# Kernel tuning notes

Measured on AMD Instinct MI355X. Metric: run time of the kernel, lower is better.

The kernel has to match this reference:

```python
import jax, jax.numpy as jnp
import numpy as np

N = 8000        # nodes
DIN = 128       # input feature dim
DOUT = 256      # internal width (dout=128 doubled by agg='weightedmean')
HEADS = 4
MAXD = 32       # max out-degree
NEG = -1e30


def setup_inputs() -> dict:
    key = jax.random.key(0)
    ks = jax.random.split(key, 12)
    # deterministic irregular degrees: 8..32, mean 20 -> m = 160000 edges
    degs = 8 + (np.arange(N) % 25)
    m = int(degs.sum())
    e0 = np.repeat(np.arange(N), degs).astype(np.int32)        # sorted source ids
    starts = np.cumsum(degs) - degs
    pos = (np.arange(m) - np.repeat(starts, degs)).astype(np.int32)  # slot within group
    rng = np.random.default_rng(0)
    e1 = rng.integers(0, N, m).astype(np.int32)                # destination ids
    p = lambda k, sh: jax.random.normal(k, sh, jnp.float32) * 0.05
    return {
        "x": jax.random.normal(ks[0], (N, DIN), jnp.float32),
        "Wc": p(ks[1], (DOUT, 2 * DIN)), "bc": p(ks[2], (DOUT,)),
        "Wq": p(ks[3], (DOUT, DOUT)), "bq": p(ks[4], (DOUT,)),
        "Wk": p(ks[5], (DOUT, DOUT)), "bk": p(ks[6], (DOUT,)),
        "Wv": p(ks[7], (DOUT, DOUT)), "bv": p(ks[8], (DOUT,)),
        "Wo": p(ks[9], (DOUT, DOUT)), "bo": p(ks[10], (DOUT,)),
        "e0": jnp.asarray(e0), "e1": jnp.asarray(e1), "pos": jnp.asarray(pos),
        "max_deg": MAXD,
    }


def reference(x, Wc, bc, Wq, bq, Wk, bk, Wv, bv, Wo, bo, e0, e1, pos, max_deg):
    n = x.shape[0]
    m = e0.shape[0]
    H = HEADS
    dh = DOUT // H                      # head dim (64)
    # gather-concat-MLP: per-edge features
    ex = jnp.concatenate([x[e0], x[e1]], axis=1)             # [m, 2*din]
    ex = jax.nn.gelu(ex @ Wc.T + bc, approximate=False)       # [m, DOUT]
    # to_dense_batch: group edges by source node (e0 is sorted)
    dense = jnp.zeros((n, max_deg, DOUT), ex.dtype).at[e0, pos].set(ex)
    mask = jnp.zeros((n, max_deg), bool).at[e0, pos].set(True)
    # standard multi-head self-attention per node-group with key padding mask
    scale = 1.0 / jnp.sqrt(jnp.asarray(dh, ex.dtype))
    q = ((dense @ Wq.T + bq) * scale).reshape(n, max_deg, H, dh)
    k = (dense @ Wk.T + bk).reshape(n, max_deg, H, dh)
    v = (dense @ Wv.T + bv).reshape(n, max_deg, H, dh)
    scores = jnp.einsum('nqhd,nkhd->nhqk', q, k)              # [n,H,D,D]
    scores = jnp.where(mask[:, None, None, :], scores, NEG)
    attn = jax.nn.softmax(scores, axis=-1)
    out = jnp.einsum('nhqk,nkhd->nqhd', attn, v).reshape(n, max_deg, DOUT)
    out = out @ Wo.T + bo
    h = jax.nn.gelu(out[e0, pos], approximate=False)          # back to [m, DOUT]
    # weightedmean aggregation: per-head value/gate split + scatter softmax on e0
    h = h.reshape(m, H, 2, dh // 2)                           # [m,H,2,32]
    logits = h[:, :, 1].mean(axis=-1)                         # [m,H]
    gmax = jax.ops.segment_max(logits, e0, num_segments=n)    # [n,H]
    ew = jnp.exp(logits - gmax[e0])
    denom = jax.ops.segment_sum(ew, e0, num_segments=n)
    alpha = ew / denom[e0]                                    # [m,H]
    contrib = (h[:, :, 0] * alpha[:, :, None]).reshape(m, -1) # [m, H*32]
    return jax.ops.segment_sum(contrib, e1, num_segments=n)   # [n, 128]
```

## Files before the change

### kernel.cpp

```cpp
#include <hip/hip_runtime.h>
#include <math.h>

typedef unsigned short ushort_t;
typedef __attribute__((ext_vector_type(8))) short short8;
typedef __attribute__((ext_vector_type(4))) short short4_t;
typedef __attribute__((ext_vector_type(4))) float f32x4;

#define MFMA_BF16(a,b,c) __builtin_amdgcn_mfma_f32_16x16x32_bf16((a),(b),(c),0,0,0)

__device__ __forceinline__ ushort_t f2bf(float f){
  union { float f; unsigned int i; } v; v.f = f;
  unsigned int r = v.i + 0x7fffu + ((v.i >> 16) & 1u);
  return (ushort_t)(r >> 16);
}
__device__ __forceinline__ float gelu_f(float x){
  float z  = x * 0.70710678118654752f;
  float az = fabsf(z);
  float t  = __builtin_amdgcn_rcpf(1.0f + 0.3275911f * az);
  float p  = t * (0.254829592f + t * (-0.284496736f + t * (1.421413741f
             + t * (-1.453152027f + t * 1.061405429f))));
  float e  = __expf(-az * az);
  float er = 1.0f - p * e;
  er = copysignf(er, z);
  return 0.5f * x * (1.0f + er);
}
__device__ __forceinline__ short8 cvt8(const float* __restrict__ p){
  f32x4 a = *(const f32x4*)p;
  f32x4 b = *(const f32x4*)(p + 4);
  short8 t;
#pragma unroll
  for (int j = 0; j < 4; ++j) { t[j] = (short)f2bf(a[j]); t[4 + j] = (short)f2bf(b[j]); }
  return t;
}

__global__ void k_prep(const int* __restrict__ e0, const int* __restrict__ pos,
                       int m, int* __restrict__ startp, int* __restrict__ degp){
  int i = blockIdx.x * 256 + threadIdx.x;
  if (i >= m) return;
  int s = e0[i];
  if (pos[i] == 0) startp[s] = i;
  if (i == m - 1 || e0[i + 1] != s) degp[s] = pos[i] + 1;
}

__global__ void k_wcvt(const float* __restrict__ Wc, const float* __restrict__ Wq,
                       const float* __restrict__ Wk, const float* __restrict__ Wv,
                       const float* __restrict__ Wo, ushort_t* __restrict__ wb){
  int i = blockIdx.x * 256 + threadIdx.x;
  if (i >= 5 * 65536) return;
  int s = i >> 16, off = i & 65535;
  const float* src = (s == 0) ? Wc : (s == 1) ? Wq : (s == 2) ? Wk : (s == 3) ? Wv : Wo;
  wb[i] = f2bf(src[off]);
}

template<bool WB>
__global__ __launch_bounds__(256, 1) void k_fused5(
    const float* __restrict__ x,
    const ushort_t* __restrict__ wb,
    const float* __restrict__ Wcf, const float* __restrict__ bc,
    const float* __restrict__ Wqf, const float* __restrict__ bq,
    const float* __restrict__ Wkf, const float* __restrict__ bk,
    const float* __restrict__ Wvf, const float* __restrict__ bv,
    const float* __restrict__ Wof, const float* __restrict__ bo,
    const int* __restrict__ e1,
    const int* __restrict__ startp, const int* __restrict__ degp,
    float* __restrict__ dout, int n)
{
  __shared__ __align__(16) ushort_t sX[64 * 264];
  __shared__ __align__(16) ushort_t sS[4 * 1440];

  const int tid = threadIdx.x;
  const int w = tid >> 6, lane = tid & 63;
  const int g = lane >> 4, li = lane & 15;
  const int colbase = w * 64;
  ushort_t* myS = &sS[w * 1440];

  int st2[2], dg2[2], nodev[2];
#pragma unroll
  for (int nd = 0; nd < 2; ++nd) {
    int node = blockIdx.x * 2 + nd;
    nodev[nd] = min(node, n - 1);
    if (node < n) { st2[nd] = startp[node]; dg2[nd] = degp[node]; }
    else { st2[nd] = 0; dg2[nd] = 0; }
  }
  if (dg2[0] <= 0 && dg2[1] <= 0) return;

  {
    int r = tid >> 2, seg = tid & 3;
    int nd0 = r >> 5, rin0 = r & 31;
    int dn = (dg2[nd0] > 0) ? e1[st2[nd0] + min(rin0, dg2[nd0] - 1)] : 0;
    const float* s = x + (size_t)dn * 128 + seg * 32;
    ushort_t* xd = &sX[r * 136 + seg * 32];
    *(short8*)(xd)      = cvt8(s);      *(short8*)(xd + 8)  = cvt8(s + 8);
    *(short8*)(xd + 16) = cvt8(s + 16); *(short8*)(xd + 24) = cvt8(s + 24);
    if (tid < 32) {
      int nd = tid >> 4, j = tid & 15;
      *(short8*)&sX[8704 + nd * 128 + j * 8] = cvt8(x + (size_t)nodev[nd] * 128 + j * 8);
    }
  }
  __syncthreads();

  {
    f32x4 acc[4][4];
#pragma unroll
    for (int a = 0; a < 4; ++a)
#pragma unroll
      for (int b = 0; b < 4; ++b) acc[a][b] = (f32x4){0.f,0.f,0.f,0.f};
#pragma unroll
    for (int ks = 0; ks < 8; ++ks) {
      short8 bf[4];
#pragma unroll
      for (int nf = 0; nf < 4; ++nf) {
        int off = (colbase + nf * 16 + li) * 256 + ks * 32 + g * 8;
        bf[nf] = WB ? *(const short8*)(wb + off) : cvt8(Wcf + off);
      }
      short8 af[4];
      if (ks < 4) {
        int k0 = ks * 32 + g * 8;
#pragma unroll
        for (int mt = 0; mt < 4; ++mt)
          af[mt] = *(const short8*)&sX[8704 + (mt >> 1) * 128 + k0];
      } else {
#pragma unroll
        for (int mt = 0; mt < 4; ++mt)
          af[mt] = *(const short8*)&sX[(mt * 16 + li) * 136 + (ks - 4) * 32 + g * 8];
      }
#pragma unroll
      for (int nf = 0; nf < 4; ++nf)
#pragma unroll
        for (int mt = 0; mt < 4; ++mt)
          acc[mt][nf] = MFMA_BF16(af[mt], bf[nf], acc[mt][nf]);
    }
    __syncthreads();
#pragma unroll
    for (int nf = 0; nf < 4; ++nf) {
      int col = colbase + nf * 16 + li;
      float b = bc[col];
#pragma unroll
      for (int mt = 0; mt < 4; ++mt)
#pragma unroll
        for (int r = 0; r < 4; ++r)
          sX[(mt * 16 + g * 4 + r) * 264 + col] = f2bf(gelu_f(acc[mt][nf][r] + b));
    }
  }
  __syncthreads();

  short8 qa[2][2][2], kbf[2][2][2];
  {
    f32x4 acc[4][4];
#pragma unroll
    for (int a = 0; a < 4; ++a)
#pragma unroll
      for (int b = 0; b < 4; ++b) acc[a][b] = (f32x4){0.f,0.f,0.f,0.f};
#pragma unroll
    for (int ks = 0; ks < 8; ++ks) {
      short8 bf[4];
#pragma unroll
      for (int nf = 0; nf < 4; ++nf) {
        int off = (colbase + nf * 16 + li) * 256 + ks * 32 + g * 8;
        bf[nf] = WB ? *(const short8*)(wb + 65536 + off) : cvt8(Wqf + off);
      }
      short8 af[4];
#pragma unroll
      for (int mt = 0; mt < 4; ++mt)
        af[mt] = *(const short8*)&sX[(mt * 16 + li) * 264 + ks * 32 + g * 8];
#pragma unroll
      for (int nf = 0; nf < 4; ++nf)
#pragma unroll
        for (int mt = 0; mt < 4; ++mt)
          acc[mt][nf] = MFMA_BF16(af[mt], bf[nf], acc[mt][nf]);
    }
    float bqv[4];
#pragma unroll
    for (int nf = 0; nf < 4; ++nf) bqv[nf] = bq[colbase + nf * 16 + li];
#pragma unroll
    for (int nd = 0; nd < 2; ++nd)
#pragma unroll
      for (int t = 0; t < 2; ++t) {
        int mt = nd * 2 + t;
#pragma unroll
        for (int nf = 0; nf < 4; ++nf)
#pragma unroll
          for (int r = 0; r < 4; ++r)
            myS[(g * 4 + r) * 72 + nf * 16 + li] = f2bf((acc[mt][nf][r] + bqv[nf]) * 0.125f);
#pragma unroll
        for (int k2 = 0; k2 < 2; ++k2)
          qa[nd][t][k2] = *(const short8*)&myS[li * 72 + k2 * 32 + g * 8];
      }
  }
  {
    f32x4 acc[4][4];
#pragma unroll
    for (int a = 0; a < 4; ++a)
#pragma unroll
      for (int b = 0; b < 4; ++b) acc[a][b] = (f32x4){0.f,0.f,0.f,0.f};
#pragma unroll
    for (int ks = 0; ks < 8; ++ks) {
      short8 bf[4];
#pragma unroll
      for (int nf = 0; nf < 4; ++nf) {
        int off = (colbase + nf * 16 + li) * 256 + ks * 32 + g * 8;
        bf[nf] = WB ? *(const short8*)(wb + 2 * 65536 + off) : cvt8(Wkf + off);
      }
      short8 af[4];
#pragma unroll
      for (int mt = 0; mt < 4; ++mt)
        af[mt] = *(const short8*)&sX[(mt * 16 + li) * 264 + ks * 32 + g * 8];
#pragma unroll
      for (int nf = 0; nf < 4; ++nf)
#pragma unroll
        for (int mt = 0; mt < 4; ++mt)
          acc[mt][nf] = MFMA_BF16(af[mt], bf[nf], acc[mt][nf]);
    }
    float bkv[4];
#pragma unroll
    for (int nf = 0; nf < 4; ++nf) bkv[nf] = bk[colbase + nf * 16 + li];
#pragma unroll
    for (int nd = 0; nd < 2; ++nd)
#pragma unroll
      for (int t = 0; t < 2; ++t) {
        int mt = nd * 2 + t;
#pragma unroll
        for (int nf = 0; nf < 4; ++nf)
#pragma unroll
          for (int r = 0; r < 4; ++r)
            myS[(g * 4 + r) * 72 + nf * 16 + li] = f2bf(acc[mt][nf][r] + bkv[nf]);
#pragma unroll
        for (int k2 = 0; k2 < 2; ++k2)
          kbf[nd][t][k2] = *(const short8*)&myS[li * 72 + k2 * 32 + g * 8];
      }
  }
  short8 pa[2][2];
#pragma unroll
  for (int nd = 0; nd < 2; ++nd) {
    const int dgn = dg2[nd];
    f32x4 sc[2][2];
#pragma unroll
    for (int a = 0; a < 2; ++a)
#pragma unroll
      for (int b = 0; b < 2; ++b) sc[a][b] = (f32x4){0.f,0.f,0.f,0.f};
#pragma unroll
    for (int k2 = 0; k2 < 2; ++k2)
#pragma unroll
      for (int mt = 0; mt < 2; ++mt)
#pragma unroll
        for (int nt = 0; nt < 2; ++nt)
          sc[mt][nt] = MFMA_BF16(qa[nd][mt][k2], kbf[nd][nt][k2], sc[mt][nt]);
#pragma unroll
    for (int mt = 0; mt < 2; ++mt) {
#pragma unroll
      for (int nt = 0; nt < 2; ++nt) {
        bool ok = (nt * 16 + li) < dgn;
#pragma unroll
        for (int r = 0; r < 4; ++r) sc[mt][nt][r] = ok ? sc[mt][nt][r] : -1e30f;
      }
#pragma unroll
      for (int r = 0; r < 4; ++r) {
        float mx = fmaxf(sc[mt][0][r], sc[mt][1][r]);
#pragma unroll
        for (int d = 1; d < 16; d <<= 1) mx = fmaxf(mx, __shfl_xor(mx, d));
        float s0 = __expf(sc[mt][0][r] - mx);
        float s1 = __expf(sc[mt][1][r] - mx);
        float sum = s0 + s1;
#pragma unroll
        for (int d = 1; d < 16; d <<= 1) sum += __shfl_xor(sum, d);
        float inv = __builtin_amdgcn_rcpf(sum);
        sc[mt][0][r] = s0 * inv;
        sc[mt][1][r] = s1 * inv;
      }
    }
#pragma unroll
    for (int mt = 0; mt < 2; ++mt)
#pragma unroll
      for (int nt = 0; nt < 2; ++nt)
#pragma unroll
        for (int r = 0; r < 4; ++r)
          myS[(mt * 16 + g * 4 + r) * 36 + nt * 16 + li] = f2bf(sc[mt][nt][r]);
#pragma unroll
    for (int t = 0; t < 2; ++t)
      pa[nd][t] = *(const short8*)&myS[(t * 16 + li) * 36 + g * 8];
  }
  {
    f32x4 acc[4][4];
#pragma unroll
    for (int a = 0; a < 4; ++a)
#pragma unroll
      for (int b = 0; b < 4; ++b) acc[a][b] = (f32x4){0.f,0.f,0.f,0.f};
#pragma unroll
    for (int ks = 0; ks < 8; ++ks) {
      short8 bf[4];
#pragma unroll
      for (int nf = 0; nf < 4; ++nf) {
        int off = (colbase + nf * 16 + li) * 256 + ks * 32 + g * 8;
        bf[nf] = WB ? *(const short8*)(wb + 3 * 65536 + off) : cvt8(Wvf + off);
      }
      short8 af[4];
#pragma unroll
      for (int mt = 0; mt < 4; ++mt)
        af[mt] = *(const short8*)&sX[(mt * 16 + li) * 264 + ks * 32 + g * 8];
#pragma unroll
      for (int nf = 0; nf < 4; ++nf)
#pragma unroll
        for (int mt = 0; mt < 4; ++mt)
          acc[mt][nf] = MFMA_BF16(af[mt], bf[nf], acc[mt][nf]);
    }
    __syncthreads();
    float bvv[4];
#pragma unroll
    for (int nf = 0; nf < 4; ++nf) bvv[nf] = bv[colbase + nf * 16 + li];
#pragma unroll
    for (int nd = 0; nd < 2; ++nd) {
      short8 vbf[4];
#pragma unroll
      for (int c2 = 0; c2 < 2; ++c2) {
#pragma unroll
        for (int nh = 0; nh < 2; ++nh) {
          int nf = c2 * 2 + nh;
#pragma unroll
          for (int t = 0; t < 2; ++t) {
            int mt = nd * 2 + t;
#pragma unroll
            for (int r = 0; r < 4; ++r)
              myS[(nh * 16 + li) * 40 + t * 16 + g * 4 + r] = f2bf(acc[mt][nf][r] + bvv[nf]);
          }
        }
#pragma unroll
        for (int nh = 0; nh < 2; ++nh)
          vbf[c2 * 2 + nh] = *(const short8*)&myS[(nh * 16 + li) * 40 + g * 8];
      }
      f32x4 o[2][4];
#pragma unroll
      for (int a = 0; a < 2; ++a)
#pragma unroll
        for (int b = 0; b < 4; ++b) o[a][b] = (f32x4){0.f,0.f,0.f,0.f};
#pragma unroll
      for (int nf = 0; nf < 4; ++nf)
#pragma unroll
        for (int t = 0; t < 2; ++t) o[t][nf] = MFMA_BF16(pa[nd][t], vbf[nf], o[t][nf]);
#pragma unroll
      for (int t = 0; t < 2; ++t)
#pragma unroll
        for (int nf = 0; nf < 4; ++nf)
#pragma unroll
          for (int r = 0; r < 4; ++r)
            sX[((nd * 2 + t) * 16 + g * 4 + r) * 264 + colbase + nf * 16 + li] = f2bf(o[t][nf][r]);
    }
  }
  __syncthreads();

  {
    f32x4 acc[4][4];
#pragma unroll
    for (int a = 0; a < 4; ++a)
#pragma unroll
      for (int b = 0; b < 4; ++b) acc[a][b] = (f32x4){0.f,0.f,0.f,0.f};
#pragma unroll
    for (int ks = 0; ks < 8; ++ks) {
      short8 bf[4];
#pragma unroll
      for (int nf = 0; nf < 4; ++nf) {
        int off = (colbase + nf * 16 + li) * 256 + ks * 32 + g * 8;
        bf[nf] = WB ? *(const short8*)(wb + 4 * 65536 + off) : cvt8(Wof + off);
      }
      short8 af[4];
#pragma unroll
      for (int mt = 0; mt < 4; ++mt)
        af[mt] = *(const short8*)&sX[(mt * 16 + li) * 264 + ks * 32 + g * 8];
#pragma unroll
      for (int nf = 0; nf < 4; ++nf)
#pragma unroll
        for (int mt = 0; mt < 4; ++mt)
          acc[mt][nf] = MFMA_BF16(af[mt], bf[nf], acc[mt][nf]);
    }
#pragma unroll
    for (int nf = 0; nf < 4; ++nf) {
      float b = bo[colbase + nf * 16 + li];
#pragma unroll
      for (int mt = 0; mt < 4; ++mt)
#pragma unroll
        for (int r = 0; r < 4; ++r) acc[mt][nf][r] = gelu_f(acc[mt][nf][r] + b);
    }
    float lp[4][4];
#pragma unroll
    for (int mt = 0; mt < 4; ++mt)
#pragma unroll
      for (int r = 0; r < 4; ++r) lp[mt][r] = acc[mt][2][r] + acc[mt][3][r];
#pragma unroll
    for (int d = 1; d < 16; d <<= 1)
#pragma unroll
      for (int mt = 0; mt < 4; ++mt)
#pragma unroll
        for (int r = 0; r < 4; ++r) lp[mt][r] += __shfl_xor(lp[mt][r], d);
#pragma unroll
    for (int nd = 0; nd < 2; ++nd) {
      const int dgn = dg2[nd], stn = st2[nd];
      float ml[2][4], mx = -1e30f;
#pragma unroll
      for (int mt2 = 0; mt2 < 2; ++mt2)
#pragma unroll
        for (int r = 0; r < 4; ++r) {
          int rin = mt2 * 16 + g * 4 + r;
          ml[mt2][r] = (rin < dgn) ? lp[nd * 2 + mt2][r] * (1.f / 32.f) : -1e30f;
          mx = fmaxf(mx, ml[mt2][r]);
        }
      mx = fmaxf(mx, __shfl_xor(mx, 16));
      mx = fmaxf(mx, __shfl_xor(mx, 32));
      float ee[2][4], ss = 0.f;
#pragma unroll
      for (int mt2 = 0; mt2 < 2; ++mt2)
#pragma unroll
        for (int r = 0; r < 4; ++r) {
          int rin = mt2 * 16 + g * 4 + r;
          ee[mt2][r] = (rin < dgn) ? __expf(ml[mt2][r] - mx) : 0.f;
          ss += ee[mt2][r];
        }
      ss += __shfl_xor(ss, 16);
      ss += __shfl_xor(ss, 32);
      float inv = __builtin_amdgcn_rcpf(ss);
#pragma unroll
      for (int mt2 = 0; mt2 < 2; ++mt2)
#pragma unroll
        for (int r = 0; r < 4; ++r) {
          int rin = mt2 * 16 + g * 4 + r;
          if (rin < dgn) {
            int eo = e1[stn + rin];
            float a = ee[mt2][r] * inv;
            atomicAdd(&dout[(size_t)eo * 128 + w * 32 + li],      acc[nd * 2 + mt2][0][r] * a);
            atomicAdd(&dout[(size_t)eo * 128 + w * 32 + 16 + li], acc[nd * 2 + mt2][1][r] * a);
          }
        }
    }
  }
}

extern "C" void kernel_launch(void* const* d_in, const int* in_sizes, int n_in,
                              void* d_out, int out_size, void* d_ws, size_t ws_size,
                              hipStream_t stream) {
  (void)n_in;
  const float* x  = (const float*)d_in[0];
  const float* Wc = (const float*)d_in[1];
  const float* bc = (const float*)d_in[2];
  const float* Wq = (const float*)d_in[3];
  const float* bq = (const float*)d_in[4];
  const float* Wk = (const float*)d_in[5];
  const float* bk = (const float*)d_in[6];
  const float* Wv = (const float*)d_in[7];
  const float* bv = (const float*)d_in[8];
  const float* Wo = (const float*)d_in[9];
  const float* bo = (const float*)d_in[10];
  const int* e0  = (const int*)d_in[11];
  const int* e1  = (const int*)d_in[12];
  const int* pos = (const int*)d_in[13];
  const int m = in_sizes[11];
  const int n = in_sizes[0] / 128;

  const size_t WBYTES = (size_t)5 * 65536 * sizeof(ushort_t);
  const bool use_wb = ws_size >= WBYTES + (size_t)n * 2 * sizeof(int);

  ushort_t* wb = (ushort_t*)d_ws;
  int* startp = use_wb ? (int*)((char*)d_ws + WBYTES) : (int*)d_ws;
  int* degp = startp + n;

  hipMemsetAsync(d_out, 0, (size_t)out_size * sizeof(float), stream);
  hipMemsetAsync(startp, 0, (size_t)n * 2 * sizeof(int), stream);

  k_prep<<<(m + 255) / 256, 256, 0, stream>>>(e0, pos, m, startp, degp);
  const int nb = (n + 1) / 2;
  if (use_wb) {
    k_wcvt<<<(5 * 65536 + 255) / 256, 256, 0, stream>>>(Wc, Wq, Wk, Wv, Wo, wb);
    k_fused5<true><<<nb, 256, 0, stream>>>(x, wb, Wc, bc, Wq, bq, Wk, bk, Wv, bv, Wo, bo,
                                           e1, startp, degp, (float*)d_out, n);
  } else {
    k_fused5<false><<<nb, 256, 0, stream>>>(x, nullptr, Wc, bc, Wq, bq, Wk, bk, Wv, bv, Wo, bo,
                                            e1, startp, degp, (float*)d_out, n);
  }
}
```

Before: 510.7 us.

## Process three nodes per block and pre-convert x to bf16 once

```diff
diff --git a/kernel.cpp b/kernel.cpp
--- a/kernel.cpp
+++ b/kernel.cpp
@@ -3,10 +3,14 @@
 
 typedef unsigned short ushort_t;
 typedef __attribute__((ext_vector_type(8))) short short8;
-typedef __attribute__((ext_vector_type(4))) short short4_t;
 typedef __attribute__((ext_vector_type(4))) float f32x4;
 
 #define MFMA_BF16(a,b,c) __builtin_amdgcn_mfma_f32_16x16x32_bf16((a),(b),(c),0,0,0)
+
+#define NN 3
+#define RT (2*NN)
+#define ROWS (32*NN)
+#define SRC_OFF (ROWS*136)
 
 __device__ __forceinline__ ushort_t f2bf(float f){
   union { float f; unsigned int i; } v; v.f = f;
@@ -51,10 +55,15 @@
   const float* src = (s == 0) ? Wc : (s == 1) ? Wq : (s == 2) ? Wk : (s == 3) ? Wv : Wo;
   wb[i] = f2bf(src[off]);
 }
+__global__ void k_xcvt(const float* __restrict__ x, ushort_t* __restrict__ xb, int total){
+  int i = blockIdx.x * 256 + threadIdx.x;
+  if (i < total) xb[i] = f2bf(x[i]);
+}
 
 template<bool WB>
-__global__ __launch_bounds__(256, 1) void k_fused5(
+__global__ __launch_bounds__(256, 1) void k_fused6(
     const float* __restrict__ x,
+    const ushort_t* __restrict__ xb,
     const ushort_t* __restrict__ wb,
     const float* __restrict__ Wcf, const float* __restrict__ bc,
     const float* __restrict__ Wqf, const float* __restrict__ bq,
@@ -65,7 +74,7 @@
     const int* __restrict__ startp, const int* __restrict__ degp,
     float* __restrict__ dout, int n)
 {
-  __shared__ __align__(16) ushort_t sX[64 * 264];
+  __shared__ __align__(16) ushort_t sX[ROWS * 264];
   __shared__ __align__(16) ushort_t sS[4 * 1440];
 
   const int tid = threadIdx.x;
@@ -74,35 +83,45 @@
   const int colbase = w * 64;
   ushort_t* myS = &sS[w * 1440];
 
-  int st2[2], dg2[2], nodev[2];
-#pragma unroll
-  for (int nd = 0; nd < 2; ++nd) {
-    int node = blockIdx.x * 2 + nd;
+  int st2[NN], dg2[NN], nodev[NN];
+#pragma unroll
+  for (int nd = 0; nd < NN; ++nd) {
+    int node = blockIdx.x * NN + nd;
     nodev[nd] = min(node, n - 1);
     if (node < n) { st2[nd] = startp[node]; dg2[nd] = degp[node]; }
     else { st2[nd] = 0; dg2[nd] = 0; }
   }
-  if (dg2[0] <= 0 && dg2[1] <= 0) return;
+  { bool any = false;
+#pragma unroll
+    for (int nd = 0; nd < NN; ++nd) any |= (dg2[nd] > 0);
+    if (!any) return; }
+
+  for (int c = tid; c < ROWS * 4; c += 256) {
+    int r0 = c >> 2, seg = c & 3;
+    int nd0 = r0 >> 5, rin0 = r0 & 31;
+    int dn = (dg2[nd0] > 0) ? e1[st2[nd0] + min(rin0, dg2[nd0] - 1)] : 0;
+    ushort_t* d = &sX[r0 * 136 + seg * 32];
+    if (WB) {
+      const ushort_t* s = xb + (size_t)dn * 128 + seg * 32;
+      *(short8*)(d)      = *(const short8*)(s);      *(short8*)(d + 8)  = *(const short8*)(s + 8);
+      *(short8*)(d + 16) = *(const short8*)(s + 16); *(short8*)(d + 24) = *(const short8*)(s + 24);
+    } else {
+      const float* s = x + (size_t)dn * 128 + seg * 32;
+      *(short8*)(d)      = cvt8(s);      *(short8*)(d + 8)  = cvt8(s + 8);
+      *(short8*)(d + 16) = cvt8(s + 16); *(short8*)(d + 24) = cvt8(s + 24);
+    }
+  }
+  if (tid < NN * 16) {
+    int nd = tid >> 4, j = tid & 15;
+    if (WB) *(short8*)&sX[SRC_OFF + nd * 128 + j * 8] = *(const short8*)(xb + (size_t)nodev[nd] * 128 + j * 8);
+    else    *(short8*)&sX[SRC_OFF + nd * 128 + j * 8] = cvt8(x + (size_t)nodev[nd] * 128 + j * 8);
+  }
+  __syncthreads();
 
   {
-    int r = tid >> 2, seg = tid & 3;
-    int nd0 = r >> 5, rin0 = r & 31;
-    int dn = (dg2[nd0] > 0) ? e1[st2[nd0] + min(rin0, dg2[nd0] - 1)] : 0;
-    const float* s = x + (size_t)dn * 128 + seg * 32;
-    ushort_t* xd = &sX[r * 136 + seg * 32];
-    *(short8*)(xd)      = cvt8(s);      *(short8*)(xd + 8)  = cvt8(s + 8);
-    *(short8*)(xd + 16) = cvt8(s + 16); *(short8*)(xd + 24) = cvt8(s + 24);
-    if (tid < 32) {
-      int nd = tid >> 4, j = tid & 15;
-      *(short8*)&sX[8704 + nd * 128 + j * 8] = cvt8(x + (size_t)nodev[nd] * 128 + j * 8);
-    }
-  }
-  __syncthreads();
-
-  {
-    f32x4 acc[4][4];
-#pragma unroll
-    for (int a = 0; a < 4; ++a)
+    f32x4 acc[RT][4];
+#pragma unroll
+    for (int a = 0; a < RT; ++a)
 #pragma unroll
       for (int b = 0; b < 4; ++b) acc[a][b] = (f32x4){0.f,0.f,0.f,0.f};
 #pragma unroll
@@ -113,21 +132,21 @@
         int off = (colbase + nf * 16 + li) * 256 + ks * 32 + g * 8;
         bf[nf] = WB ? *(const short8*)(wb + off) : cvt8(Wcf + off);
       }
-      short8 af[4];
+      short8 af[RT];
       if (ks < 4) {
         int k0 = ks * 32 + g * 8;
 #pragma unroll
-        for (int mt = 0; mt < 4; ++mt)
-          af[mt] = *(const short8*)&sX[8704 + (mt >> 1) * 128 + k0];
+        for (int mt = 0; mt < RT; ++mt)
+          af[mt] = *(const short8*)&sX[SRC_OFF + (mt >> 1) * 128 + k0];
       } else {
 #pragma unroll
-        for (int mt = 0; mt < 4; ++mt)
+        for (int mt = 0; mt < RT; ++mt)
           af[mt] = *(const short8*)&sX[(mt * 16 + li) * 136 + (ks - 4) * 32 + g * 8];
       }
 #pragma unroll
       for (int nf = 0; nf < 4; ++nf)
 #pragma unroll
-        for (int mt = 0; mt < 4; ++mt)
+        for (int mt = 0; mt < RT; ++mt)
           acc[mt][nf] = MFMA_BF16(af[mt], bf[nf], acc[mt][nf]);
     }
     __syncthreads();
@@ -136,7 +155,7 @@
       int col = colbase + nf * 16 + li;
       float b = bc[col];
 #pragma unroll
-      for (int mt = 0; mt < 4; ++mt)
+      for (int mt = 0; mt < RT; ++mt)
 #pragma unroll
         for (int r = 0; r < 4; ++r)
           sX[(mt * 16 + g * 4 + r) * 264 + col] = f2bf(gelu_f(acc[mt][nf][r] + b));
@@ -144,11 +163,11 @@
   }
   __syncthreads();
 
-  short8 qa[2][2][2], kbf[2][2][2];
+  short8 qa[NN][2][2], kbf[NN][2][2];
   {
-    f32x4 acc[4][4];
-#pragma unroll
-    for (int a = 0; a < 4; ++a)
+    f32x4 acc[RT][4];
+#pragma unroll
+    for (int a = 0; a < RT; ++a)
 #pragma unroll
       for (int b = 0; b < 4; ++b) acc[a][b] = (f32x4){0.f,0.f,0.f,0.f};
 #pragma unroll
@@ -159,21 +178,21 @@
         int off = (colbase + nf * 16 + li) * 256 + ks * 32 + g * 8;
         bf[nf] = WB ? *(const short8*)(wb + 65536 + off) : cvt8(Wqf + off);
       }
-      short8 af[4];
-#pragma unroll
-      for (int mt = 0; mt < 4; ++mt)
+      short8 af[RT];
+#pragma unroll
+      for (int mt = 0; mt < RT; ++mt)
         af[mt] = *(const short8*)&sX[(mt * 16 + li) * 264 + ks * 32 + g * 8];
 #pragma unroll
       for (int nf = 0; nf < 4; ++nf)
 #pragma unroll
-        for (int mt = 0; mt < 4; ++mt)
+        for (int mt = 0; mt < RT; ++mt)
           acc[mt][nf] = MFMA_BF16(af[mt], bf[nf], acc[mt][nf]);
     }
     float bqv[4];
 #pragma unroll
     for (int nf = 0; nf < 4; ++nf) bqv[nf] = bq[colbase + nf * 16 + li];
 #pragma unroll
-    for (int nd = 0; nd < 2; ++nd)
+    for (int nd = 0; nd < NN; ++nd)
 #pragma unroll
       for (int t = 0; t < 2; ++t) {
         int mt = nd * 2 + t;
@@ -188,9 +207,9 @@
       }
   }
   {
-    f32x4 acc[4][4];
-#pragma unroll
-    for (int a = 0; a < 4; ++a)
+    f32x4 acc[RT][4];
+#pragma unroll
+    for (int a = 0; a < RT; ++a)
 #pragma unroll
       for (int b = 0; b < 4; ++b) acc[a][b] = (f32x4){0.f,0.f,0.f,0.f};
 #pragma unroll
@@ -201,21 +220,21 @@
         int off = (colbase + nf * 16 + li) * 256 + ks * 32 + g * 8;
         bf[nf] = WB ? *(const short8*)(wb + 2 * 65536 + off) : cvt8(Wkf + off);
       }
-      short8 af[4];
-#pragma unroll
-      for (int mt = 0; mt < 4; ++mt)
+      short8 af[RT];
+#pragma unroll
+      for (int mt = 0; mt < RT; ++mt)
         af[mt] = *(const short8*)&sX[(mt * 16 + li) * 264 + ks * 32 + g * 8];
 #pragma unroll
       for (int nf = 0; nf < 4; ++nf)
 #pragma unroll
-        for (int mt = 0; mt < 4; ++mt)
+        for (int mt = 0; mt < RT; ++mt)
           acc[mt][nf] = MFMA_BF16(af[mt], bf[nf], acc[mt][nf]);
     }
     float bkv[4];
 #pragma unroll
     for (int nf = 0; nf < 4; ++nf) bkv[nf] = bk[colbase + nf * 16 + li];
 #pragma unroll
-    for (int nd = 0; nd < 2; ++nd)
+    for (int nd = 0; nd < NN; ++nd)
 #pragma unroll
       for (int t = 0; t < 2; ++t) {
         int mt = nd * 2 + t;
@@ -229,9 +248,9 @@
           kbf[nd][t][k2] = *(const short8*)&myS[li * 72 + k2 * 32 + g * 8];
       }
   }
-  short8 pa[2][2];
-#pragma unroll
-  for (int nd = 0; nd < 2; ++nd) {
+  short8 pa[NN][2];
+#pragma unroll
+  for (int nd = 0; nd < NN; ++nd) {
     const int dgn = dg2[nd];
     f32x4 sc[2][2];
 #pragma unroll
@@ -280,9 +299,9 @@
       pa[nd][t] = *(const short8*)&myS[(t * 16 + li) * 36 + g * 8];
   }
   {
-    f32x4 acc[4][4];
-#pragma unroll
-    for (int a = 0; a < 4; ++a)
+    f32x4 acc[RT][4];
+#pragma unroll
+    for (int a = 0; a < RT; ++a)
 #pragma unroll
       for (int b = 0; b < 4; ++b) acc[a][b] = (f32x4){0.f,0.f,0.f,0.f};
 #pragma unroll
@@ -293,14 +312,14 @@
         int off = (colbase + nf * 16 + li) * 256 + ks * 32 + g * 8;
         bf[nf] = WB ? *(const short8*)(wb + 3 * 65536 + off) : cvt8(Wvf + off);
       }
-      short8 af[4];
-#pragma unroll
-      for (int mt = 0; mt < 4; ++mt)
+      short8 af[RT];
+#pragma unroll
+      for (int mt = 0; mt < RT; ++mt)
         af[mt] = *(const short8*)&sX[(mt * 16 + li) * 264 + ks * 32 + g * 8];
 #pragma unroll
       for (int nf = 0; nf < 4; ++nf)
 #pragma unroll
-        for (int mt = 0; mt < 4; ++mt)
+        for (int mt = 0; mt < RT; ++mt)
           acc[mt][nf] = MFMA_BF16(af[mt], bf[nf], acc[mt][nf]);
     }
     __syncthreads();
@@ -308,7 +327,7 @@
 #pragma unroll
     for (int nf = 0; nf < 4; ++nf) bvv[nf] = bv[colbase + nf * 16 + li];
 #pragma unroll
-    for (int nd = 0; nd < 2; ++nd) {
+    for (int nd = 0; nd < NN; ++nd) {
       short8 vbf[4];
 #pragma unroll
       for (int c2 = 0; c2 < 2; ++c2) {
@@ -348,9 +367,9 @@
   __syncthreads();
 
   {
-    f32x4 acc[4][4];
-#pragma unroll
-    for (int a = 0; a < 4; ++a)
+    f32x4 acc[RT][4];
+#pragma unroll
+    for (int a = 0; a < RT; ++a)
 #pragma unroll
       for (int b = 0; b < 4; ++b) acc[a][b] = (f32x4){0.f,0.f,0.f,0.f};
 #pragma unroll
@@ -361,37 +380,37 @@
         int off = (colbase + nf * 16 + li) * 256 + ks * 32 + g * 8;
         bf[nf] = WB ? *(const short8*)(wb + 4 * 65536 + off) : cvt8(Wof + off);
       }
-      short8 af[4];
-#pragma unroll
-      for (int mt = 0; mt < 4; ++mt)
+      short8 af[RT];
+#pragma unroll
+      for (int mt = 0; mt < RT; ++mt)
         af[mt] = *(const short8*)&sX[(mt * 16 + li) * 264 + ks * 32 + g * 8];
 #pragma unroll
       for (int nf = 0; nf < 4; ++nf)
 #pragma unroll
-        for (int mt = 0; mt < 4; ++mt)
+        for (int mt = 0; mt < RT; ++mt)
           acc[mt][nf] = MFMA_BF16(af[mt], bf[nf], acc[mt][nf]);
     }
 #pragma unroll
     for (int nf = 0; nf < 4; ++nf) {
       float b = bo[colbase + nf * 16 + li];
 #pragma unroll
-      for (int mt = 0; mt < 4; ++mt)
+      for (int mt = 0; mt < RT; ++mt)
 #pragma unroll
         for (int r = 0; r < 4; ++r) acc[mt][nf][r] = gelu_f(acc[mt][nf][r] + b);
     }
-    float lp[4][4];
-#pragma unroll
-    for (int mt = 0; mt < 4; ++mt)
+    float lp[RT][4];
+#pragma unroll
+    for (int mt = 0; mt < RT; ++mt)
 #pragma unroll
       for (int r = 0; r < 4; ++r) lp[mt][r] = acc[mt][2][r] + acc[mt][3][r];
 #pragma unroll
     for (int d = 1; d < 16; d <<= 1)
 #pragma unroll
-      for (int mt = 0; mt < 4; ++mt)
+      for (int mt = 0; mt < RT; ++mt)
 #pragma unroll
         for (int r = 0; r < 4; ++r) lp[mt][r] += __shfl_xor(lp[mt][r], d);
 #pragma unroll
-    for (int nd = 0; nd < 2; ++nd) {
+    for (int nd = 0; nd < NN; ++nd) {
       const int dgn = dg2[nd], stn = st2[nd];
       float ml[2][4], mx = -1e30f;
 #pragma unroll
@@ -454,23 +473,26 @@
   const int n = in_sizes[0] / 128;
 
   const size_t WBYTES = (size_t)5 * 65536 * sizeof(ushort_t);
-  const bool use_wb = ws_size >= WBYTES + (size_t)n * 2 * sizeof(int);
+  const size_t XBYTES = (size_t)n * 128 * sizeof(ushort_t);
+  const bool use_wb = ws_size >= WBYTES + XBYTES + (size_t)n * 2 * sizeof(int);
 
   ushort_t* wb = (ushort_t*)d_ws;
-  int* startp = use_wb ? (int*)((char*)d_ws + WBYTES) : (int*)d_ws;
+  ushort_t* xb = (ushort_t*)((char*)d_ws + WBYTES);
+  int* startp = use_wb ? (int*)((char*)d_ws + WBYTES + XBYTES) : (int*)d_ws;
   int* degp = startp + n;
 
   hipMemsetAsync(d_out, 0, (size_t)out_size * sizeof(float), stream);
   hipMemsetAsync(startp, 0, (size_t)n * 2 * sizeof(int), stream);
 
   k_prep<<<(m + 255) / 256, 256, 0, stream>>>(e0, pos, m, startp, degp);
-  const int nb = (n + 1) / 2;
+  const int nb = (n + NN - 1) / NN;
   if (use_wb) {
     k_wcvt<<<(5 * 65536 + 255) / 256, 256, 0, stream>>>(Wc, Wq, Wk, Wv, Wo, wb);
-    k_fused5<true><<<nb, 256, 0, stream>>>(x, wb, Wc, bc, Wq, bq, Wk, bk, Wv, bv, Wo, bo,
+    k_xcvt<<<(n * 128 + 255) / 256, 256, 0, stream>>>(x, xb, n * 128);
+    k_fused6<true><<<nb, 256, 0, stream>>>(x, xb, wb, Wc, bc, Wq, bq, Wk, bk, Wv, bv, Wo, bo,
                                            e1, startp, degp, (float*)d_out, n);
   } else {
-    k_fused5<false><<<nb, 256, 0, stream>>>(x, nullptr, Wc, bc, Wq, bq, Wk, bk, Wv, bv, Wo, bo,
+    k_fused6<false><<<nb, 256, 0, stream>>>(x, nullptr, nullptr, Wc, bc, Wq, bq, Wk, bk, Wv, bv, Wo, bo,
                                             e1, startp, degp, (float*)d_out, n);
   }
 }
```

Measured after the change: 630.9 us. +23.5%, slower.
